# Optimization experiments

Hardware: AMD Instinct MI355X
Metric: run time of the kernel (lower is better)

## Reference

```python
import jax, jax.numpy as jnp
import numpy as np

B, T, N1, K = 128, 512, 512, 8   # batch, steps, n_customers+1, knn_k
CAPACITY = 50.0
NEG_INF = -1e9


def setup_inputs() -> dict:
    key = jax.random.key(0)
    k0, k1, k2, k3, k4, k5 = jax.random.split(key, 6)
    psi_prime = jax.random.normal(k0, (B, N1, 2), dtype=jnp.float32)
    demands = jax.random.uniform(k1, (B, N1), dtype=jnp.float32) * 9.0 + 1.0
    demands = demands.at[:, 0].set(0.0)  # depot has zero demand
    actions = jax.random.randint(k2, (B, T), 0, N1, dtype=jnp.int32)
    knn_indices = jax.random.randint(k3, (B, N1, K), 0, N1, dtype=jnp.int32)
    Wq_w = jax.random.normal(k4, (2, 4), dtype=jnp.float32) * 0.5
    Wq_b = jax.random.normal(k5, (2,), dtype=jnp.float32) * 0.1
    lambda_param = jnp.float32(0.1)
    return {"psi_prime": psi_prime, "demands": demands, "Wq_w": Wq_w,
            "Wq_b": Wq_b, "lambda_param": lambda_param,
            "actions": actions, "knn_indices": knn_indices}


def _rollout_states(demands, actions):
    """Reconstruct the T per-step states (cur, used, vis) BEFORE each action."""
    mb, Tn = actions.shape
    n1 = demands.shape[1]
    batch = jnp.arange(mb)

    def step(carry, act_t):
        cur, used, vis = carry
        out = (cur, used, vis)  # record state before applying act_t
        at_depot = act_t == 0
        dem_t = jnp.take_along_axis(demands, act_t[:, None], axis=1)[:, 0]
        used_n = jnp.where(at_depot, 0.0, used + dem_t)
        vis_n = vis.at[batch, act_t].set(True)
        vis_n = vis_n.at[:, 0].set(False)
        return (act_t, used_n, vis_n), out

    init = (jnp.zeros((mb,), jnp.int32), jnp.zeros((mb,), jnp.float32),
            jnp.zeros((mb, n1), dtype=bool))
    _, (all_cur, all_used, all_vis) = jax.lax.scan(step, init, actions.T)
    # scan stacks over leading T axis -> move batch first
    return all_cur.T, all_used.T, jnp.transpose(all_vis, (1, 0, 2))


def _evaluate(psi_prime, demands, Wq_w, Wq_b, lambda_param, actions, knn_indices):
    mb, Tn = actions.shape
    n_cust = psi_prime.shape[1] - 1

    all_cur, all_used, all_vis = _rollout_states(demands, actions)  # [B,T],[B,T],[B,T,N1]

    remaining = CAPACITY - all_used                      # [B,T]
    cap_norm = remaining / max(CAPACITY, 1e-8)
    exceeds = demands[:, None, :] > remaining[:, :, None]  # [B,T,N1]
    mask = all_vis | exceeds
    mask = mask.at[:, :, 0].set(False)
    at_depot = all_cur == 0                               # [B,T]
    has_cust = jnp.any(~mask[:, :, 1:], axis=-1)
    mask = mask.at[:, :, 0].set(at_depot & has_cust)

    psi_curr = jnp.take_along_axis(psi_prime, all_cur[:, :, None], axis=1)  # [B,T,2]
    psi_curr = jnp.where(at_depot[:, :, None], 0.0, psi_curr)
    t_norm = jnp.arange(Tn, dtype=jnp.float32) / max(n_cust, 1)
    t_norm = jnp.broadcast_to(t_norm[None, :], (mb, Tn))
    ctx = jnp.concatenate([psi_curr, cap_norm[:, :, None], t_norm[:, :, None]], axis=-1)  # [B,T,4]

    query = ctx @ Wq_w.T + Wq_b                           # [B,T,2]
    context_scores = jnp.einsum('btd,bnd->btn', query, psi_prime)  # [B,T,N1]

    # kNN interference: per-node dot with its k nearest neighbours, summed
    neigh = psi_prime[jnp.arange(mb)[:, None, None], knn_indices]  # [B,N1,K,2]
    interf = jnp.einsum('bnd,bnkd->bn', psi_prime, neigh)          # [B,N1]

    scores = context_scores + lambda_param * interf[:, None, :]
    scores = jnp.where(mask, NEG_INF, scores)
    log_probs = jax.nn.log_softmax(scores, axis=-1)                # [B,T,N1]

    lp_new = jnp.take_along_axis(log_probs, actions[:, :, None], axis=2)[:, :, 0]  # [B,T]
    ent = -jnp.sum(jnp.exp(log_probs) * log_probs, axis=-1)        # [B,T]
    entropy = ent.mean(axis=1)                                     # [B]
    return lp_new, entropy


def reference(psi_prime, demands, Wq_w, Wq_b, lambda_param, actions, knn_indices):
    return _evaluate(psi_prime, demands, Wq_w, Wq_b, lambda_param, actions, knn_indices)
```

## Files before the change

kernel.cpp:

```cpp
#include <hip/hip_runtime.h>
#include <hip/hip_bf16.h>

#define B_  128
#define T_  512
#define N1_ 512
#define K_  8
#define CAPf 50.0f
#define NEG_INF_F (-1000000000.0f)
#define NEG_INF_L2 (-1442695040.0f)
#define L2E  1.44269504088896341f
#define LN2  0.69314718055994531f

__device__ __forceinline__ int   fi(float x) { return __float_as_int(x); }
__device__ __forceinline__ float uf(int x)   { return __int_as_float(x); }

__device__ __forceinline__ float wave_sum64(float x) {
    x += uf(__builtin_amdgcn_update_dpp(0, fi(x), 0x111, 0xF, 0xF, true));
    x += uf(__builtin_amdgcn_update_dpp(0, fi(x), 0x112, 0xF, 0xF, true));
    x += uf(__builtin_amdgcn_update_dpp(0, fi(x), 0x114, 0xF, 0xF, true));
    x += uf(__builtin_amdgcn_update_dpp(0, fi(x), 0x118, 0xF, 0xF, true));
    x += uf(__builtin_amdgcn_update_dpp(0, fi(x), 0x142, 0xA, 0xF, true));
    x += uf(__builtin_amdgcn_update_dpp(0, fi(x), 0x143, 0xC, 0xF, true));
    return uf(__builtin_amdgcn_readlane(fi(x), 63));
}
__device__ __forceinline__ float wave_max64_pos(float x) {
    x = fmaxf(x, uf(__builtin_amdgcn_update_dpp(0, fi(x), 0x111, 0xF, 0xF, true)));
    x = fmaxf(x, uf(__builtin_amdgcn_update_dpp(0, fi(x), 0x112, 0xF, 0xF, true)));
    x = fmaxf(x, uf(__builtin_amdgcn_update_dpp(0, fi(x), 0x114, 0xF, 0xF, true)));
    x = fmaxf(x, uf(__builtin_amdgcn_update_dpp(0, fi(x), 0x118, 0xF, 0xF, true)));
    x = fmaxf(x, uf(__builtin_amdgcn_update_dpp(0, fi(x), 0x142, 0xA, 0xF, true)));
    x = fmaxf(x, uf(__builtin_amdgcn_update_dpp(0, fi(x), 0x143, 0xC, 0xF, true)));
    return uf(__builtin_amdgcn_readlane(fi(x), 63));
}

__global__ __launch_bounds__(256) void prep_kernel(
    const float* __restrict__ psi,
    const float* __restrict__ demands,
    const float* __restrict__ lambda_p,
    const int*   __restrict__ actions,
    const int*   __restrict__ knn,
    float4* __restrict__ ws_pk,
    int*    __restrict__ ws_fv,
    float*  __restrict__ ws_used)
{
    __shared__ float2 psi_l[N1_];
    __shared__ float  dem_l[N1_];
    __shared__ int    fv_l[N1_];
    __shared__ int    act_l[T_];
    __shared__ float2 md_l[T_];

    const int b   = blockIdx.x;
    const int tid = threadIdx.x;

    const float2* psi2 = (const float2*)psi;
    for (int i = tid; i < N1_; i += 256) {
        psi_l[i] = psi2[b * N1_ + i];
        dem_l[i] = demands[b * N1_ + i];
        fv_l[i]  = 0x7fffffff;
    }
    for (int t = tid; t < T_; t += 256) act_l[t] = actions[b * T_ + t];
    __syncthreads();

    for (int t = tid; t < T_; t += 256) {
        int a = act_l[t];
        atomicMin(&fv_l[a], t);
        float d = dem_l[a];
        md_l[t] = (a == 0) ? make_float2(0.0f, 0.0f) : make_float2(1.0f, d);
    }
    __syncthreads();

    if (tid == 0) {
        float u = 0.0f;
        #pragma unroll 8
        for (int t = 0; t < T_; ++t) {
            ws_used[b * T_ + t] = u;
            float2 md = md_l[t];
            u = fmaf(md.x, u, md.y);
        }
    } else if (tid >= 64) {
        const float lam = (*lambda_p) * L2E;
        for (int n = tid - 64; n < N1_; n += 192) {
            float2 p = psi_l[n];
            const int4* kk = (const int4*)(knn + ((size_t)b * N1_ + n) * K_);
            int4 k0 = kk[0], k1 = kk[1];
            int ks[8] = {k0.x, k0.y, k0.z, k0.w, k1.x, k1.y, k1.z, k1.w};
            float acc = 0.0f;
            #pragma unroll
            for (int k = 0; k < 8; ++k) {
                float2 q = psi_l[ks[k]];
                acc = fmaf(p.x, q.x, acc);
                acc = fmaf(p.y, q.y, acc);
            }
            ws_pk[b * N1_ + n] = make_float4(p.x, p.y, lam * acc, dem_l[n]);
        }
    }
    __syncthreads();
    for (int n = tid; n < N1_; n += 256) ws_fv[b * N1_ + n] = fv_l[n];
}

__global__ __launch_bounds__(512) void main_kernel(
    const float*  __restrict__ Wq_w,
    const float*  __restrict__ Wq_b,
    const int*    __restrict__ actions,
    const float4* __restrict__ ws_pk,
    const int*    __restrict__ ws_fv,
    const float*  __restrict__ ws_used,
    float* __restrict__ out_lp,
    float* __restrict__ out_ent)
{
    __shared__ float4 pk_l[N1_];
    __shared__ int    fv_l[N1_];
    __shared__ float  used_s[128];
    __shared__ int    act_s[129];
    __shared__ float  went[8];

    const int bid     = blockIdx.x;
    const int b       = bid >> 2;
    const int quarter = bid & 3;
    const int t_base  = quarter * 128;
    const int tid     = threadIdx.x;
    const int wave    = tid >> 6;
    const int lane    = tid & 63;

    if (tid < N1_) {
        pk_l[tid] = ws_pk[b * N1_ + tid];
        fv_l[tid] = ws_fv[b * N1_ + tid];
    }
    if (tid < 128) used_s[tid] = ws_used[b * T_ + t_base + tid];
    if (tid < 129) {
        int tt = t_base - 1 + tid;
        act_s[tid] = (tt < 0) ? 0 : actions[b * T_ + tt];
    }
    const float W00 = Wq_w[0], W01 = Wq_w[1], W02 = Wq_w[2], W03 = Wq_w[3];
    const float W10 = Wq_w[4], W11 = Wq_w[5], W12 = Wq_w[6], W13 = Wq_w[7];
    const float bq0 = Wq_b[0], bq1 = Wq_b[1];
    __syncthreads();

    float ent_acc = 0.0f;

    #pragma unroll 1
    for (int rr = 0; rr < 8; ++rr) {
        const int iA = wave * 16 + rr * 2;
        const int iB = iA + 1;
        const int tA = t_base + iA;
        const int tB = t_base + iB;
        const int curA = (tA == 0) ? 0 : act_s[iA];
        const int curB = act_s[iB];
        const int aA = act_s[iA + 1];
        const int aB = act_s[iB + 1];
        const float remA = CAPf - used_s[iA];
        const float remB = CAPf - used_s[iB];
        const bool depA = (curA == 0);
        const bool depB = (curB == 0);

        float4 pcA = pk_l[curA];
        float4 pcB = pk_l[curB];
        const float pcxA = depA ? 0.0f : pcA.x, pcyA = depA ? 0.0f : pcA.y;
        const float pcxB = depB ? 0.0f : pcB.x, pcyB = depB ? 0.0f : pcB.y;

        const float capA = remA * (1.0f / CAPf), capB = remB * (1.0f / CAPf);
        const float tnA = (float)tA * (1.0f / 511.0f);
        const float tnB = (float)tB * (1.0f / 511.0f);

        const float q0A = fmaf(pcxA, W00, fmaf(pcyA, W01, fmaf(capA, W02, fmaf(tnA, W03, bq0)))) * L2E;
        const float q1A = fmaf(pcxA, W10, fmaf(pcyA, W11, fmaf(capA, W12, fmaf(tnA, W13, bq1)))) * L2E;
        const float q0B = fmaf(pcxB, W00, fmaf(pcyB, W01, fmaf(capB, W02, fmaf(tnB, W03, bq0)))) * L2E;
        const float q1B = fmaf(pcxB, W10, fmaf(pcyB, W11, fmaf(capB, W12, fmaf(tnB, W13, bq1)))) * L2E;

        float sA[8], sB[8];
        bool avA = false, avB = false;
        #pragma unroll
        for (int j = 0; j < 8; ++j) {
            const int n = j * 64 + lane;
            const float4 P = pk_l[n];
            const int   fv = fv_l[n];
            float scA = fmaf(q0A, P.x, fmaf(q1A, P.y, P.z));
            float scB = fmaf(q0B, P.x, fmaf(q1B, P.y, P.z));
            if (n != 0) {
                bool mA = (fv < tA) | (P.w > remA);
                bool mB = (fv < tB) | (P.w > remB);
                avA |= !mA;  avB |= !mB;
                scA = mA ? NEG_INF_L2 : scA;
                scB = mB ? NEG_INF_L2 : scB;
            }
            sA[j] = scA;  sB[j] = scB;
        }

        const bool hasA = __any((int)avA);
        const bool hasB = __any((int)avB);
        if (lane == 0 && depA && hasA) sA[0] = NEG_INF_L2;
        if (lane == 0 && depB && hasB) sB[0] = NEG_INF_L2;

        float preA = fmaxf(fmaxf(fmaxf(sA[0], sA[1]), fmaxf(sA[2], sA[3])),
                           fmaxf(fmaxf(sA[4], sA[5]), fmaxf(sA[6], sA[7])));
        float preB = fmaxf(fmaxf(fmaxf(sB[0], sB[1]), fmaxf(sB[2], sB[3])),
                           fmaxf(fmaxf(sB[4], sB[5]), fmaxf(sB[6], sB[7])));
        const float mxA = wave_max64_pos(preA + 2048.0f) - 2048.0f;
        const float mxB = wave_max64_pos(preB + 2048.0f) - 2048.0f;

        float S1A = 0.0f, S2A = 0.0f, S1B = 0.0f, S2B = 0.0f;
        #pragma unroll
        for (int j = 0; j < 8; ++j) {
            float eA = __builtin_amdgcn_exp2f(sA[j] - mxA);
            float eB = __builtin_amdgcn_exp2f(sB[j] - mxB);
            S1A += eA;  S2A = fmaf(eA, sA[j], S2A);
            S1B += eB;  S2B = fmaf(eB, sB[j], S2B);
        }
        S1A = wave_sum64(S1A);  S2A = wave_sum64(S2A);
        S1B = wave_sum64(S1B);  S2B = wave_sum64(S2B);

        const float lgA = __builtin_amdgcn_logf(S1A);
        const float lgB = __builtin_amdgcn_logf(S1B);

        const int jaA = aA >> 6, jaB = aB >> 6;
        float svA = sA[0], svB = sB[0];
        svA = (jaA == 1) ? sA[1] : svA;  svB = (jaB == 1) ? sB[1] : svB;
        svA = (jaA == 2) ? sA[2] : svA;  svB = (jaB == 2) ? sB[2] : svB;
        svA = (jaA == 3) ? sA[3] : svA;  svB = (jaB == 3) ? sB[3] : svB;
        svA = (jaA == 4) ? sA[4] : svA;  svB = (jaB == 4) ? sB[4] : svB;
        svA = (jaA == 5) ? sA[5] : svA;  svB = (jaB == 5) ? sB[5] : svB;
        svA = (jaA == 6) ? sA[6] : svA;  svB = (jaB == 6) ? sB[6] : svB;
        svA = (jaA == 7) ? sA[7] : svA;  svB = (jaB == 7) ? sB[7] : svB;
        const float s_aA = uf(__builtin_amdgcn_readlane(fi(svA), aA & 63));
        const float s_aB = uf(__builtin_amdgcn_readlane(fi(svB), aB & 63));

        if (lane == 0) {
            out_lp[b * T_ + tA] = LN2 * ((s_aA - mxA) - lgA);
            out_lp[b * T_ + tB] = LN2 * ((s_aB - mxB) - lgB);
        }
        ent_acc += ((mxA + lgA) - __fdividef(S2A, S1A))
                 + ((mxB + lgB) - __fdividef(S2B, S1B));
    }

    if (lane == 0) went[wave] = ent_acc;
    __syncthreads();
    if (tid == 0) {
        float s = ((went[0] + went[1]) + (went[2] + went[3]))
                + ((went[4] + went[5]) + (went[6] + went[7]));
        atomicAdd(&out_ent[b], s * (LN2 / 512.0f));
    }
}

extern "C" void kernel_launch(void* const* d_in, const int* in_sizes, int n_in,
                              void* d_out, int out_size, void* d_ws, size_t ws_size,
                              hipStream_t stream) {
    const float* psi      = (const float*)d_in[0];
    const float* demands  = (const float*)d_in[1];
    const float* Wq_w     = (const float*)d_in[2];
    const float* Wq_b     = (const float*)d_in[3];
    const float* lam      = (const float*)d_in[4];
    const int*   actions  = (const int*)d_in[5];
    const int*   knn      = (const int*)d_in[6];

    float* out_lp  = (float*)d_out;
    float* out_ent = out_lp + (size_t)B_ * T_;

    float4* ws_pk  = (float4*)d_ws;
    int*    ws_fv  = (int*)  ((char*)d_ws + (size_t)B_ * N1_ * 16);
    float*  ws_used= (float*)((char*)d_ws + (size_t)B_ * N1_ * 20);

    prep_kernel<<<B_, 256, 0, stream>>>(psi, demands, lam, actions, knn,
                                        ws_pk, ws_fv, ws_used);
    main_kernel<<<B_ * 4, 512, 0, stream>>>(Wq_w, Wq_b, actions,
                                            ws_pk, ws_fv, ws_used,
                                            out_lp, out_ent);
}
```

Baseline: 97.24 us.

## Fuse prep and main kernels, recomputing per-batch prep inside each block

The separate prep kernel is merged into the main kernel. Each of the four blocks per batch now rebuilds the packed node data, first-visit indices, kNN interference and capacity prefix in shared memory, instead of reading them back from a global workspace. Per-lane node data and first-visit values are also hoisted into registers before the step loop. This removes a launch and the workspace round trip, at the cost of redundant prep work in every block and a serial prefix scan of up to 512 steps on one thread.

```diff
diff --git a/kernel.cpp b/kernel.cpp
--- a/kernel.cpp
+++ b/kernel.cpp
@@ -6,7 +6,6 @@
 #define N1_ 512
 #define K_  8
 #define CAPf 50.0f
-#define NEG_INF_F (-1000000000.0f)
 #define NEG_INF_L2 (-1442695040.0f)
 #define L2E  1.44269504088896341f
 #define LN2  0.69314718055994531f
@@ -33,103 +32,80 @@
     return uf(__builtin_amdgcn_readlane(fi(x), 63));
 }
 
-__global__ __launch_bounds__(256) void prep_kernel(
+__global__ __launch_bounds__(512) void fused_kernel(
     const float* __restrict__ psi,
     const float* __restrict__ demands,
+    const float* __restrict__ Wq_w,
+    const float* __restrict__ Wq_b,
     const float* __restrict__ lambda_p,
     const int*   __restrict__ actions,
     const int*   __restrict__ knn,
-    float4* __restrict__ ws_pk,
-    int*    __restrict__ ws_fv,
-    float*  __restrict__ ws_used)
-{
-    __shared__ float2 psi_l[N1_];
-    __shared__ float  dem_l[N1_];
-    __shared__ int    fv_l[N1_];
-    __shared__ int    act_l[T_];
-    __shared__ float2 md_l[T_];
-
-    const int b   = blockIdx.x;
-    const int tid = threadIdx.x;
-
-    const float2* psi2 = (const float2*)psi;
-    for (int i = tid; i < N1_; i += 256) {
-        psi_l[i] = psi2[b * N1_ + i];
-        dem_l[i] = demands[b * N1_ + i];
-        fv_l[i]  = 0x7fffffff;
-    }
-    for (int t = tid; t < T_; t += 256) act_l[t] = actions[b * T_ + t];
-    __syncthreads();
-
-    for (int t = tid; t < T_; t += 256) {
-        int a = act_l[t];
-        atomicMin(&fv_l[a], t);
-        float d = dem_l[a];
-        md_l[t] = (a == 0) ? make_float2(0.0f, 0.0f) : make_float2(1.0f, d);
-    }
-    __syncthreads();
-
-    if (tid == 0) {
-        float u = 0.0f;
-        #pragma unroll 8
-        for (int t = 0; t < T_; ++t) {
-            ws_used[b * T_ + t] = u;
-            float2 md = md_l[t];
-            u = fmaf(md.x, u, md.y);
-        }
-    } else if (tid >= 64) {
-        const float lam = (*lambda_p) * L2E;
-        for (int n = tid - 64; n < N1_; n += 192) {
-            float2 p = psi_l[n];
-            const int4* kk = (const int4*)(knn + ((size_t)b * N1_ + n) * K_);
-            int4 k0 = kk[0], k1 = kk[1];
-            int ks[8] = {k0.x, k0.y, k0.z, k0.w, k1.x, k1.y, k1.z, k1.w};
-            float acc = 0.0f;
-            #pragma unroll
-            for (int k = 0; k < 8; ++k) {
-                float2 q = psi_l[ks[k]];
-                acc = fmaf(p.x, q.x, acc);
-                acc = fmaf(p.y, q.y, acc);
-            }
-            ws_pk[b * N1_ + n] = make_float4(p.x, p.y, lam * acc, dem_l[n]);
-        }
-    }
-    __syncthreads();
-    for (int n = tid; n < N1_; n += 256) ws_fv[b * N1_ + n] = fv_l[n];
-}
-
-__global__ __launch_bounds__(512) void main_kernel(
-    const float*  __restrict__ Wq_w,
-    const float*  __restrict__ Wq_b,
-    const int*    __restrict__ actions,
-    const float4* __restrict__ ws_pk,
-    const int*    __restrict__ ws_fv,
-    const float*  __restrict__ ws_used,
     float* __restrict__ out_lp,
     float* __restrict__ out_ent)
 {
     __shared__ float4 pk_l[N1_];
     __shared__ int    fv_l[N1_];
+    __shared__ int    act_l[T_];
+    __shared__ float2 md_l[T_];
     __shared__ float  used_s[128];
-    __shared__ int    act_s[129];
     __shared__ float  went[8];
 
     const int bid     = blockIdx.x;
     const int b       = bid >> 2;
     const int quarter = bid & 3;
     const int t_base  = quarter * 128;
+    const int t_end   = t_base + 128;
     const int tid     = threadIdx.x;
     const int wave    = tid >> 6;
     const int lane    = tid & 63;
 
+    const float2* psi2 = (const float2*)psi;
     if (tid < N1_) {
-        pk_l[tid] = ws_pk[b * N1_ + tid];
-        fv_l[tid] = ws_fv[b * N1_ + tid];
-    }
-    if (tid < 128) used_s[tid] = ws_used[b * T_ + t_base + tid];
-    if (tid < 129) {
-        int tt = t_base - 1 + tid;
-        act_s[tid] = (tt < 0) ? 0 : actions[b * T_ + tt];
+        float2 p = psi2[b * N1_ + tid];
+        pk_l[tid] = make_float4(p.x, p.y, 0.0f, demands[b * N1_ + tid]);
+        fv_l[tid] = 0x7fffffff;
+        act_l[tid] = actions[b * T_ + tid];
+    }
+    __syncthreads();
+
+    {
+        const int t = tid;
+        int a = act_l[t];
+        atomicMin(&fv_l[a], t);
+        float d = pk_l[a].w;
+        md_l[t] = (a == 0) ? make_float2(0.0f, 0.0f) : make_float2(1.0f, d);
+
+        const float lam = (*lambda_p) * L2E;
+        const int n = tid;
+        float px = pk_l[n].x, py = pk_l[n].y;
+        const int4* kk = (const int4*)(knn + ((size_t)b * N1_ + n) * K_);
+        int4 k0 = kk[0], k1 = kk[1];
+        int ks[8] = {k0.x, k0.y, k0.z, k0.w, k1.x, k1.y, k1.z, k1.w};
+        float acc = 0.0f;
+        #pragma unroll
+        for (int k = 0; k < 8; ++k) {
+            acc = fmaf(px, pk_l[ks[k]].x, acc);
+            acc = fmaf(py, pk_l[ks[k]].y, acc);
+        }
+        pk_l[n].z = lam * acc;
+    }
+    __syncthreads();
+
+    if (tid == 0) {
+        float u = 0.0f;
+        #pragma unroll 8
+        for (int t = 0; t < t_end; ++t) {
+            if (t >= t_base) used_s[t - t_base] = u;
+            float2 md = md_l[t];
+            u = fmaf(md.x, u, md.y);
+        }
+    }
+    float4 pk[8];
+    int    fvr[8];
+    #pragma unroll
+    for (int j = 0; j < 8; ++j) {
+        pk[j]  = pk_l[j * 64 + lane];
+        fvr[j] = fv_l[j * 64 + lane];
     }
     const float W00 = Wq_w[0], W01 = Wq_w[1], W02 = Wq_w[2], W03 = Wq_w[3];
     const float W10 = Wq_w[4], W11 = Wq_w[5], W12 = Wq_w[6], W13 = Wq_w[7];
@@ -144,10 +120,10 @@
         const int iB = iA + 1;
         const int tA = t_base + iA;
         const int tB = t_base + iB;
-        const int curA = (tA == 0) ? 0 : act_s[iA];
-        const int curB = act_s[iB];
-        const int aA = act_s[iA + 1];
-        const int aB = act_s[iB + 1];
+        const int curA = (tA == 0) ? 0 : act_l[tA - 1];
+        const int curB = act_l[tB - 1];
+        const int aA = act_l[tA];
+        const int aB = act_l[tB];
         const float remA = CAPf - used_s[iA];
         const float remB = CAPf - used_s[iB];
         const bool depA = (curA == 0);
@@ -172,13 +148,11 @@
         #pragma unroll
         for (int j = 0; j < 8; ++j) {
             const int n = j * 64 + lane;
-            const float4 P = pk_l[n];
-            const int   fv = fv_l[n];
-            float scA = fmaf(q0A, P.x, fmaf(q1A, P.y, P.z));
-            float scB = fmaf(q0B, P.x, fmaf(q1B, P.y, P.z));
+            float scA = fmaf(q0A, pk[j].x, fmaf(q1A, pk[j].y, pk[j].z));
+            float scB = fmaf(q0B, pk[j].x, fmaf(q1B, pk[j].y, pk[j].z));
             if (n != 0) {
-                bool mA = (fv < tA) | (P.w > remA);
-                bool mB = (fv < tB) | (P.w > remB);
+                bool mA = (fvr[j] < tA) | (pk[j].w > remA);
+                bool mB = (fvr[j] < tB) | (pk[j].w > remB);
                 avA |= !mA;  avB |= !mB;
                 scA = mA ? NEG_INF_L2 : scA;
                 scB = mB ? NEG_INF_L2 : scB;
@@ -255,13 +229,6 @@
     float* out_lp  = (float*)d_out;
     float* out_ent = out_lp + (size_t)B_ * T_;
 
-    float4* ws_pk  = (float4*)d_ws;
-    int*    ws_fv  = (int*)  ((char*)d_ws + (size_t)B_ * N1_ * 16);
-    float*  ws_used= (float*)((char*)d_ws + (size_t)B_ * N1_ * 20);
-
-    prep_kernel<<<B_, 256, 0, stream>>>(psi, demands, lam, actions, knn,
-                                        ws_pk, ws_fv, ws_used);
-    main_kernel<<<B_ * 4, 512, 0, stream>>>(Wq_w, Wq_b, actions,
-                                            ws_pk, ws_fv, ws_used,
-                                            out_lp, out_ent);
-}
+    fused_kernel<<<B_ * 4, 512, 0, stream>>>(psi, demands, Wq_w, Wq_b, lam,
+                                             actions, knn, out_lp, out_ent);
+}
```

New measurement: 111.0 us. 1.14x slower.
